# Kernel optimization log

Hardware: AMD Instinct MI355X
Metric: run time of the kernel (lower is better)

## Reference

```python
import jax, jax.numpy as jnp
import numpy as np

E, C, M, H, O = 8, 4096, 1024, 4096, 1024  # experts, capacity, model_dim, hidden, output_dim

def setup_inputs() -> dict:
    key = jax.random.key(0)
    k1, k2, k3, k4, k5 = jax.random.split(key, 5)
    s1 = 1.0 / np.sqrt(M)
    s2 = 1.0 / np.sqrt(H)
    return {
        "x": jax.random.normal(k1, (E, C, M), dtype=jnp.float32),
        "fc1_w": jax.random.normal(k2, (E, M, H), dtype=jnp.float32) * s1,
        "fc1_b": jax.random.normal(k3, (E, H), dtype=jnp.float32) * s1,
        "fc2_w": jax.random.normal(k4, (E, H, O), dtype=jnp.float32) * s2,
        "fc2_b": jax.random.normal(k5, (E, O), dtype=jnp.float32) * s2,
    }

def reference(x, fc1_w, fc1_b, fc2_w, fc2_b):
    # grouped GEMM over experts: [E,C,M] @ [E,M,H] -> [E,C,H]
    y = jnp.einsum('ecm,emh->ech', x, fc1_w) + fc1_b[:, None, :]
    y = jax.nn.relu(y)  # default activation_fn
    # [E,C,H] @ [E,H,O] -> [E,C,O]
    out = jnp.einsum('ech,eho->eco', y, fc2_w) + fc2_b[:, None, :]
    return out
```

## Files before the change

### kernel.cpp

```cpp
#include <hip/hip_runtime.h>
#include <hip/hip_bf16.h>


typedef __attribute__((ext_vector_type(8))) short short8;
typedef __attribute__((ext_vector_type(4))) float f32x4;

typedef const __attribute__((address_space(1))) void GV;
typedef __attribute__((address_space(3))) void LV;

#define BAR()                                                                  \
    do {                                                                       \
        asm volatile("" ::: "memory");                                         \
        __builtin_amdgcn_s_barrier();                                          \
        asm volatile("" ::: "memory");                                         \
    } while (0)

__device__ inline ushort f2bf_rne(float f) {
    union { float f; unsigned u; } v; v.f = f;
    unsigned u = v.u;
    u += 0x7FFFu + ((u >> 16) & 1u);
    return (ushort)(u >> 16);
}

__global__ __launch_bounds__(256) void convert_bf16(
    const float* __restrict__ in, ushort* __restrict__ out, long n) {
    long i = ((long)blockIdx.x * 256 + threadIdx.x) * 8;
    if (i + 7 >= n) return;
    float4 v0 = *(const float4*)&in[i];
    float4 v1 = *(const float4*)&in[i + 4];
    short8 o;
    o[0] = f2bf_rne(v0.x); o[1] = f2bf_rne(v0.y);
    o[2] = f2bf_rne(v0.z); o[3] = f2bf_rne(v0.w);
    o[4] = f2bf_rne(v1.x); o[5] = f2bf_rne(v1.y);
    o[6] = f2bf_rne(v1.z); o[7] = f2bf_rne(v1.w);
    *(short8*)&out[i] = o;
}

__global__ __launch_bounds__(256) void transpose_convert(
    const float* __restrict__ in, ushort* __restrict__ out, int R, int Cn) {
    __shared__ float tile[64][65];
    const int e  = blockIdx.z;
    const float* ine  = in  + (size_t)e * R * Cn;
    ushort*      oute = out + (size_t)e * R * Cn;
    const int r0 = blockIdx.y * 64;
    const int c0 = blockIdx.x * 64;
    const int t  = threadIdx.x;
#pragma unroll
    for (int i = 0; i < 4; ++i) {
        int idx = i * 256 + t;
        int ir  = idx >> 4;
        int icc = (idx & 15) * 4;
        float4 v = *(const float4*)&ine[(size_t)(r0 + ir) * Cn + c0 + icc];
        tile[ir][icc + 0] = v.x; tile[ir][icc + 1] = v.y;
        tile[ir][icc + 2] = v.z; tile[ir][icc + 3] = v.w;
    }
    __syncthreads();
#pragma unroll
    for (int i = 0; i < 2; ++i) {
        int idx = i * 256 + t;
        int ic  = idx >> 3;
        int ir0 = (idx & 7) * 8;
        short8 o;
#pragma unroll
        for (int j = 0; j < 8; ++j) o[j] = f2bf_rne(tile[ir0 + j][ic]);
        *(short8*)&oute[(size_t)(c0 + ic) * R + r0 + ir0] = o;
    }
}


#define MFMA_Q(QM, QN)                                                         \
    do {                                                                       \
        _Pragma("unroll")                                                      \
        for (int kh = 0; kh < 2; ++kh)                                         \
            _Pragma("unroll")                                                  \
            for (int mf = 0; mf < 4; ++mf)                                     \
                _Pragma("unroll")                                              \
                for (int nf = 0; nf < 2; ++nf)                                 \
                    acc[(QM) * 4 + mf][(QN) * 2 + nf] =                        \
                        __builtin_amdgcn_mfma_f32_16x16x32_bf16(               \
                            a[(QM) * 4 + mf][kh], b[nf][kh],                   \
                            acc[(QM) * 4 + mf][(QN) * 2 + nf], 0, 0, 0);       \
    } while (0)

#define STAGE(P0, P1_, HOFF, LBASE, TG)                                        \
    do {                                                                       \
        const int _tg = (TG);                                                  \
        if (_tg < NTt) {                                                       \
            const size_t _k = (size_t)_tg * 64;                                \
            __builtin_amdgcn_global_load_lds((GV*)((P0) + (HOFF) + _k),        \
                (LV*)&smem[(LBASE) + d0], 16, 0, 0);                           \
            __builtin_amdgcn_global_load_lds((GV*)((P1_) + (HOFF) + _k),       \
                (LV*)&smem[(LBASE) + d1], 16, 0, 0);                           \
        }                                                                      \
    } while (0)

template <bool RELU_BF16_OUT, int MT, int NTILES, int K, int N>
__global__ __launch_bounds__(512, 2) void gemm8p(
    const ushort* __restrict__ A, const ushort* __restrict__ Bt,
    const float* __restrict__ bias, void* __restrict__ out) {
    __shared__ ushort smem[65536];
    constexpr int NTt = K / 64;
    constexpr int STC = NTILES / 4;

    const int pid = blockIdx.x;
    const int e   = pid & 7;
    const int idx = pid >> 3;
    const int s  = idx >> 4, wi = idx & 15;
    const int by = (s / STC) * 4 + (wi >> 2);
    const int bx = (s % STC) * 4 + (wi & 3);
    const int m0 = by * 256, n0 = bx * 256;

    const ushort* Ae = A  + (size_t)e * 4096 * K;
    const ushort* Be = Bt + (size_t)e * N * K;
    const float*  be = bias + (size_t)e * N;

    const int t    = threadIdx.x;
    const int w    = t >> 6, l = t & 63;
    const int wm   = w >> 2;
    const int wn   = w & 3;
    const int lrow = l & 15, q = l >> 4;
    const int swz  = (lrow & 7) << 3;

    const int r0s = w * 16 + (l >> 3);
    const int r1s = r0s + 8;
    const int c0s = ((l & 7) ^ (r0s & 7)) << 3;
    const int c1s = ((l & 7) ^ (r1s & 7)) << 3;
    const int d0  = w * 1024 + l * 8;
    const int d1  = d0 + 512;

    const ushort* pa0 = Ae + (size_t)(m0 + r0s) * K + c0s;
    const ushort* pa1 = Ae + (size_t)(m0 + r1s) * K + c1s;
    const ushort* pb0 = Be + (size_t)(n0 + r0s) * K + c0s;
    const ushort* pb1 = Be + (size_t)(n0 + r1s) * K + c1s;

    float bv[4];
#pragma unroll
    for (int nf = 0; nf < 4; ++nf) bv[nf] = be[n0 + wn * 64 + nf * 16 + lrow];
    asm volatile("s_waitcnt vmcnt(0)" ::: "memory");

    STAGE(pa0, pa1, (size_t)0,       0,             0);
    STAGE(pa0, pa1, (size_t)128 * K, 8192,          0);
    STAGE(pb0, pb1, (size_t)0,       16384,         0);
    STAGE(pb0, pb1, (size_t)128 * K, 16384 + 8192,  0);
    STAGE(pa0, pa1, (size_t)0,       32768,         1);
    STAGE(pa0, pa1, (size_t)128 * K, 32768 + 8192,  1);
    asm volatile("s_waitcnt vmcnt(4)" ::: "memory");
    BAR();

    short8 a[8][2], b[2][2];
    f32x4 acc[8][4] = {};

    for (int ti = 0; ti < NTt; ++ti) {
        const int buf  = ti & 1;
        const int obuf = buf ^ 1;
        const ushort* Ab = &smem[buf * 32768 + wm * 8192];
        const ushort* Bb = &smem[buf * 32768 + 16384 + (wn >> 1) * 8192 +
                                 (wn & 1) * 4096];

#pragma unroll
        for (int mf = 0; mf < 4; ++mf)
#pragma unroll
            for (int kh = 0; kh < 2; ++kh)
                a[mf][kh] = *(const short8*)
                    &Ab[(mf * 16 + lrow) * 64 + ((kh * 32 + q * 8) ^ swz)];
#pragma unroll
        for (int nf = 0; nf < 2; ++nf)
#pragma unroll
            for (int kh = 0; kh < 2; ++kh)
                b[nf][kh] = *(const short8*)
                    &Bb[(nf * 16 + lrow) * 64 + ((kh * 32 + q * 8) ^ swz)];
        STAGE(pb0, pb1, (size_t)0, obuf * 32768 + 16384, ti + 1);
        BAR();
        __builtin_amdgcn_s_setprio(1);
        MFMA_Q(0, 0);
        __builtin_amdgcn_s_setprio(0);
        BAR();

#pragma unroll
        for (int mf = 0; mf < 4; ++mf)
#pragma unroll
            for (int kh = 0; kh < 2; ++kh)
                a[4 + mf][kh] = *(const short8*)
                    &Ab[((4 + mf) * 16 + lrow) * 64 + ((kh * 32 + q * 8) ^ swz)];
        STAGE(pb0, pb1, (size_t)128 * K, obuf * 32768 + 16384 + 8192, ti + 1);
        BAR();
        __builtin_amdgcn_s_setprio(1);
        MFMA_Q(1, 0);
        __builtin_amdgcn_s_setprio(0);
        BAR();

#pragma unroll
        for (int nf = 0; nf < 2; ++nf)
#pragma unroll
            for (int kh = 0; kh < 2; ++kh)
                b[nf][kh] = *(const short8*)
                    &Bb[((2 + nf) * 16 + lrow) * 64 + ((kh * 32 + q * 8) ^ swz)];
        STAGE(pa0, pa1, (size_t)0, buf * 32768, ti + 2);
        BAR();
        __builtin_amdgcn_s_setprio(1);
        MFMA_Q(1, 1);
        __builtin_amdgcn_s_setprio(0);
        BAR();

        STAGE(pa0, pa1, (size_t)128 * K, buf * 32768 + 8192, ti + 2);
        BAR();
        __builtin_amdgcn_s_setprio(1);
        MFMA_Q(0, 1);
        __builtin_amdgcn_s_setprio(0);
        if (ti < NTt - 2) {
            asm volatile("s_waitcnt vmcnt(4)" ::: "memory");
        } else if (ti == NTt - 2) {
            asm volatile("s_waitcnt vmcnt(0)" ::: "memory");
        }
        BAR();
    }

    const size_t obase = (size_t)e * 4096 * N;
#pragma unroll
    for (int mf = 0; mf < 8; ++mf) {
#pragma unroll
        for (int nf = 0; nf < 4; ++nf) {
            const int gn = n0 + wn * 64 + nf * 16 + lrow;
#pragma unroll
            for (int rr = 0; rr < 4; ++rr) {
                const int gm = m0 + wm * 128 + mf * 16 + q * 4 + rr;
                float v = acc[mf][nf][rr] + bv[nf];
                if (RELU_BF16_OUT) {
                    v = fmaxf(v, 0.f);
                    ((ushort*)out)[obase + (size_t)gm * N + gn] = f2bf_rne(v);
                } else {
                    ((float*)out)[obase + (size_t)gm * N + gn] = v;
                }
            }
        }
    }
}

extern "C" void kernel_launch(void* const* d_in, const int* in_sizes, int n_in,
                              void* d_out, int out_size, void* d_ws, size_t ws_size,
                              hipStream_t stream) {
    const int E = 8, C = 4096, M = 1024, H = 4096, O = 1024;
    const float* x  = (const float*)d_in[0];
    const float* w1 = (const float*)d_in[1];
    const float* b1 = (const float*)d_in[2];
    const float* w2 = (const float*)d_in[3];
    const float* b2 = (const float*)d_in[4];
    float* out = (float*)d_out;

    ushort* x_bf = (ushort*)d_ws;
    ushort* w1t  = x_bf + (size_t)E * C * M;
    ushort* w2t  = w1t;
    ushort* y_bf = w1t + (size_t)E * M * H;

    const long nx = (long)E * C * M;
    convert_bf16<<<(nx / 8 + 255) / 256, 256, 0, stream>>>(x, x_bf, nx);
    transpose_convert<<<dim3(H / 64, M / 64, E), 256, 0, stream>>>(w1, w1t, M, H);
    gemm8p<true, 16, 16, 1024, 4096><<<16 * 16 * 8, 512, 0, stream>>>(
        x_bf, w1t, b1, (void*)y_bf);
    transpose_convert<<<dim3(O / 64, H / 64, E), 256, 0, stream>>>(w2, w2t, H, O);
    gemm8p<false, 16, 4, 4096, 1024><<<16 * 4 * 8, 512, 0, stream>>>(
        y_bf, w2t, b2, (void*)out);
}
```

Baseline: 903.4 us.

## Ping-pong A fragment registers to prefetch next K-tile during final MFMA burst

```diff
diff --git a/kernel.cpp b/kernel.cpp
--- a/kernel.cpp
+++ b/kernel.cpp
@@ -68,7 +68,7 @@
 }
 
 
-#define MFMA_Q(QM, QN)                                                         \
+#define MFMA_BURST(AARR, ABASE, QN)                                            \
     do {                                                                       \
         _Pragma("unroll")                                                      \
         for (int kh = 0; kh < 2; ++kh)                                         \
@@ -76,10 +76,10 @@
             for (int mf = 0; mf < 4; ++mf)                                     \
                 _Pragma("unroll")                                              \
                 for (int nf = 0; nf < 2; ++nf)                                 \
-                    acc[(QM) * 4 + mf][(QN) * 2 + nf] =                        \
+                    acc[(ABASE) + mf][(QN) * 2 + nf] =                         \
                         __builtin_amdgcn_mfma_f32_16x16x32_bf16(               \
-                            a[(QM) * 4 + mf][kh], b[nf][kh],                   \
-                            acc[(QM) * 4 + mf][(QN) * 2 + nf], 0, 0, 0);       \
+                            AARR[mf][kh], b[nf][kh],                           \
+                            acc[(ABASE) + mf][(QN) * 2 + nf], 0, 0, 0);        \
     } while (0)
 
 #define STAGE(P0, P1_, HOFF, LBASE, TG)                                        \
@@ -94,12 +94,93 @@
         }                                                                      \
     } while (0)
 
+#define TILE_BODY(TI, CUR, HI, PBUF)                                           \
+  do {                                                                         \
+    const int ti_ = (TI);                                                      \
+    const ushort* Ab_  = &smem[(PBUF) * 32768 + wm * 8192];                    \
+    const ushort* Bb_  = &smem[(PBUF) * 32768 + 16384 + (wn >> 1) * 8192 +     \
+                               (wn & 1) * 4096];                               \
+    const ushort* AbN_ = &smem[((PBUF) ^ 1) * 32768 + wm * 8192];              \
+            \
+    _Pragma("unroll")                                                          \
+    for (int nf = 0; nf < 2; ++nf)                                             \
+        _Pragma("unroll")                                                      \
+        for (int kh = 0; kh < 2; ++kh)                                         \
+            b[nf][kh] = *(const short8*)                                       \
+                &Bb_[(nf * 16 + lrow) * 64 + ((kh * 32 + q * 8) ^ swz)];       \
+    STAGE(pb0, pb1, (size_t)0, ((PBUF) ^ 1) * 32768 + 16384, ti_ + 1);         \
+    BAR();                                                                     \
+    asm volatile("s_waitcnt lgkmcnt(0)" ::: "memory");                         \
+    __builtin_amdgcn_sched_barrier(0);                                         \
+    __builtin_amdgcn_s_setprio(1);                                             \
+    MFMA_BURST(CUR, 0, 0);                                                     \
+    __builtin_amdgcn_s_setprio(0);                                             \
+    BAR();                                                                     \
+        \
+    _Pragma("unroll")                                                          \
+    for (int mf = 0; mf < 4; ++mf)                                             \
+        _Pragma("unroll")                                                      \
+        for (int kh = 0; kh < 2; ++kh)                                         \
+            HI[mf][kh] = *(const short8*)                                      \
+                &Ab_[((4 + mf) * 16 + lrow) * 64 + ((kh * 32 + q * 8) ^ swz)]; \
+    STAGE(pb0, pb1, (size_t)128 * K, ((PBUF) ^ 1) * 32768 + 16384 + 8192,      \
+          ti_ + 1);                                                            \
+    BAR();                                                                     \
+    asm volatile("s_waitcnt lgkmcnt(0)" ::: "memory");                         \
+    __builtin_amdgcn_sched_barrier(0);                                         \
+    __builtin_amdgcn_s_setprio(1);                                             \
+    MFMA_BURST(HI, 4, 0);                                                      \
+    __builtin_amdgcn_s_setprio(0);                                             \
+    BAR();                                                                     \
+            \
+    _Pragma("unroll")                                                          \
+    for (int nf = 0; nf < 2; ++nf)                                             \
+        _Pragma("unroll")                                                      \
+        for (int kh = 0; kh < 2; ++kh)                                         \
+            b[nf][kh] = *(const short8*)                                       \
+                &Bb_[((2 + nf) * 16 + lrow) * 64 + ((kh * 32 + q * 8) ^ swz)]; \
+    STAGE(pa0, pa1, (size_t)0, (PBUF) * 32768, ti_ + 2);                       \
+    BAR();                                                                     \
+    asm volatile("s_waitcnt lgkmcnt(0)" ::: "memory");                         \
+    __builtin_amdgcn_sched_barrier(0);                                         \
+    __builtin_amdgcn_s_setprio(1);                                             \
+    MFMA_BURST(HI, 4, 1);                                                      \
+    __builtin_amdgcn_s_setprio(0);                                             \
+    BAR();                                                                     \
+           \
+    if (ti_ + 1 < NTt) {                                                       \
+        if (ti_ < NTt - 2)                                                     \
+            asm volatile("s_waitcnt vmcnt(6)" ::: "memory");                   \
+        else                                                                   \
+            asm volatile("s_waitcnt vmcnt(4)" ::: "memory");                   \
+        _Pragma("unroll")                                                      \
+        for (int mf = 0; mf < 4; ++mf)                                         \
+            _Pragma("unroll")                                                  \
+            for (int kh = 0; kh < 2; ++kh)                                     \
+                HI[mf][kh] = *(const short8*)                                  \
+                    &AbN_[(mf * 16 + lrow) * 64 + ((kh * 32 + q * 8) ^ swz)];  \
+    }                                                                          \
+    STAGE(pa0, pa1, (size_t)128 * K, (PBUF) * 32768 + 8192, ti_ + 2);          \
+    BAR();                                                                     \
+    asm volatile("s_waitcnt lgkmcnt(0)" ::: "memory");                         \
+    __builtin_amdgcn_sched_barrier(0);                                         \
+    __builtin_amdgcn_s_setprio(1);                                             \
+    MFMA_BURST(CUR, 0, 1);                                                     \
+    __builtin_amdgcn_s_setprio(0);                                             \
+    if (ti_ < NTt - 2)                                                         \
+        asm volatile("s_waitcnt vmcnt(4)" ::: "memory");                       \
+    else if (ti_ == NTt - 2)                                                   \
+        asm volatile("s_waitcnt vmcnt(0)" ::: "memory");                       \
+    BAR();                                                                     \
+  } while (0)
+
 template <bool RELU_BF16_OUT, int MT, int NTILES, int K, int N>
 __global__ __launch_bounds__(512, 2) void gemm8p(
     const ushort* __restrict__ A, const ushort* __restrict__ Bt,
     const float* __restrict__ bias, void* __restrict__ out) {
     __shared__ ushort smem[65536];
     constexpr int NTt = K / 64;
+    static_assert(K % 64 == 0 && (NTt % 2) == 0, "need even K-tile count");
     constexpr int STC = NTILES / 4;
 
     const int pid = blockIdx.x;
@@ -147,72 +228,20 @@
     asm volatile("s_waitcnt vmcnt(4)" ::: "memory");
     BAR();
 
-    short8 a[8][2], b[2][2];
+    short8 aX[4][2], aY[4][2], b[2][2];
     f32x4 acc[8][4] = {};
 
-    for (int ti = 0; ti < NTt; ++ti) {
-        const int buf  = ti & 1;
-        const int obuf = buf ^ 1;
-        const ushort* Ab = &smem[buf * 32768 + wm * 8192];
-        const ushort* Bb = &smem[buf * 32768 + 16384 + (wn >> 1) * 8192 +
-                                 (wn & 1) * 4096];
-
-#pragma unroll
-        for (int mf = 0; mf < 4; ++mf)
-#pragma unroll
-            for (int kh = 0; kh < 2; ++kh)
-                a[mf][kh] = *(const short8*)
-                    &Ab[(mf * 16 + lrow) * 64 + ((kh * 32 + q * 8) ^ swz)];
-#pragma unroll
-        for (int nf = 0; nf < 2; ++nf)
-#pragma unroll
-            for (int kh = 0; kh < 2; ++kh)
-                b[nf][kh] = *(const short8*)
-                    &Bb[(nf * 16 + lrow) * 64 + ((kh * 32 + q * 8) ^ swz)];
-        STAGE(pb0, pb1, (size_t)0, obuf * 32768 + 16384, ti + 1);
-        BAR();
-        __builtin_amdgcn_s_setprio(1);
-        MFMA_Q(0, 0);
-        __builtin_amdgcn_s_setprio(0);
-        BAR();
-
-#pragma unroll
-        for (int mf = 0; mf < 4; ++mf)
-#pragma unroll
-            for (int kh = 0; kh < 2; ++kh)
-                a[4 + mf][kh] = *(const short8*)
-                    &Ab[((4 + mf) * 16 + lrow) * 64 + ((kh * 32 + q * 8) ^ swz)];
-        STAGE(pb0, pb1, (size_t)128 * K, obuf * 32768 + 16384 + 8192, ti + 1);
-        BAR();
-        __builtin_amdgcn_s_setprio(1);
-        MFMA_Q(1, 0);
-        __builtin_amdgcn_s_setprio(0);
-        BAR();
-
-#pragma unroll
-        for (int nf = 0; nf < 2; ++nf)
-#pragma unroll
-            for (int kh = 0; kh < 2; ++kh)
-                b[nf][kh] = *(const short8*)
-                    &Bb[((2 + nf) * 16 + lrow) * 64 + ((kh * 32 + q * 8) ^ swz)];
-        STAGE(pa0, pa1, (size_t)0, buf * 32768, ti + 2);
-        BAR();
-        __builtin_amdgcn_s_setprio(1);
-        MFMA_Q(1, 1);
-        __builtin_amdgcn_s_setprio(0);
-        BAR();
-
-        STAGE(pa0, pa1, (size_t)128 * K, buf * 32768 + 8192, ti + 2);
-        BAR();
-        __builtin_amdgcn_s_setprio(1);
-        MFMA_Q(0, 1);
-        __builtin_amdgcn_s_setprio(0);
-        if (ti < NTt - 2) {
-            asm volatile("s_waitcnt vmcnt(4)" ::: "memory");
-        } else if (ti == NTt - 2) {
-            asm volatile("s_waitcnt vmcnt(0)" ::: "memory");
-        }
-        BAR();
+#pragma unroll
+    for (int mf = 0; mf < 4; ++mf)
+#pragma unroll
+        for (int kh = 0; kh < 2; ++kh)
+            aX[mf][kh] = *(const short8*)
+                &smem[wm * 8192 + (mf * 16 + lrow) * 64 +
+                      ((kh * 32 + q * 8) ^ swz)];
+
+    for (int tt = 0; tt < NTt; tt += 2) {
+        TILE_BODY(tt,     aX, aY, 0);
+        TILE_BODY(tt + 1, aY, aX, 1);
     }
 
     const size_t obase = (size_t)e * 4096 * N;
```

Result: faster. 878.1 us (-2.8%).
